# Kernel tuning notes

Measured on AMD Instinct MI355X. Metric: run time of the kernel, lower is better.

The kernel has to match this reference:

```python
import jax, jax.numpy as jnp
import numpy as np


def setup_inputs() -> dict:
    key = jax.random.key(0)
    k1, k2 = jax.random.split(key)
    z = jax.random.normal(k1, (16, 128, 32, 32), dtype=jnp.float32)
    e = jax.random.normal(k2, (8192, 128), dtype=jnp.float32)
    log_sigma = jnp.zeros((1,), dtype=jnp.float32)  # init_log_sigma = 0.0
    return {"z": z, "e": e, "log_sigma": log_sigma}


def reference(z, e, log_sigma):
    # z: [B, C, H, W] latents; e: [M, C] codebook; log_sigma: [1]
    B, C, H, W = z.shape
    zf = jnp.transpose(z, (0, 2, 3, 1)).reshape(-1, C)  # [N, C]
    N = zf.shape[0]
    M = e.shape[0]
    T = 1.0  # latent_temp default

    # squared L2 distance via expanded dot products: ||z||^2 + ||e||^2 - 2 z.e
    z_sq = jnp.sum(zf * zf, axis=1, keepdims=True)          # [N, 1]
    e_sq = jnp.sum(e * e, axis=1)[None, :]                  # [1, M]
    dist = jnp.maximum(z_sq + e_sq - 2.0 * (zf @ e.T), 0.0)  # [N, M]

    alpha = -1.0 / (2.0 * jnp.exp(log_sigma[0]) ** 2)
    A = alpha * dist / T                                     # [N, M]

    # np.log(np.e) == 1.0 in the original
    const = 0.5 * C * (2.0 * log_sigma - 1.0)                # [1]
    lse1_loss = -jnp.mean(T * jax.nn.logsumexp(A, axis=1)) + const + jnp.log(float(M))
    lse2_loss = -jnp.mean(T * jax.nn.logsumexp(A, axis=0)) + const + jnp.log(float(N))
    return lse1_loss, lse2_loss
```

## Files before the change

### kernel.cpp

```cpp
#include <hip/hip_runtime.h>
#include <hip/hip_bf16.h>

typedef unsigned short u16;
typedef __attribute__((ext_vector_type(8))) short short8;
typedef __attribute__((ext_vector_type(4))) float float4v;

#define N_ROWS 16384
#define M_COLS 8192
#define KDIM   128
#define SHIFT  64.0f
#define STRIPES 64
#define SPLITS  16
#define TILES   8

__device__ inline u16 f2bf(float f) {
  unsigned u = __builtin_bit_cast(unsigned, f);
  unsigned r = (u + 0x7fffu + ((u >> 16) & 1u)) >> 16;
  return (u16)r;
}

__global__ void prep(const float* __restrict__ z, const float* __restrict__ e,
                     u16* __restrict__ zf, u16* __restrict__ ef,
                     float* __restrict__ zsq, float* __restrict__ esq,
                     double* __restrict__ dacc, unsigned* __restrict__ dcnt) {
  if (blockIdx.x < 512) {
    const int b = blockIdx.x >> 5, h = blockIdx.x & 31;
    __shared__ float tile[128 * 33];
    __shared__ float psum[8][32];
    const float* src = z + ((size_t)b * 128 * 32 + h) * 32;
    for (int idx = threadIdx.x; idx < 4096; idx += 256) {
      int c = idx >> 5, w = idx & 31;
      tile[c * 33 + w] = src[c * 1024 + w];
    }
    __syncthreads();
    {
      int w = threadIdx.x & 31, cg = threadIdx.x >> 5;
      float s = 0.f;
#pragma unroll
      for (int cc = 0; cc < 16; ++cc) {
        float v = tile[(cg * 16 + cc) * 33 + w];
        s = fmaf(v, v, s);
      }
      psum[cg][w] = s;
    }
    for (int idx = threadIdx.x; idx < 512; idx += 256) {
      int w = idx >> 4, g = idx & 15;
      short8 v;
#pragma unroll
      for (int cc = 0; cc < 8; ++cc) v[cc] = (short)f2bf(tile[(g * 8 + cc) * 33 + w]);
      *(short8*)&zf[((size_t)b * 1024 + h * 32 + w) * 128 + g * 8] = v;
    }
    __syncthreads();
    if (threadIdx.x < 32) {
      int w = threadIdx.x;
      float s = 0.f;
#pragma unroll
      for (int cg = 0; cg < 8; ++cg) s += psum[cg][w];
      zsq[b * 1024 + h * 32 + w] = s;
    }
  } else {
    if (blockIdx.x == 512 && threadIdx.x == 0) {
      __hip_atomic_store(&dacc[0], 0.0, __ATOMIC_RELAXED, __HIP_MEMORY_SCOPE_AGENT);
      __hip_atomic_store(&dacc[1], 0.0, __ATOMIC_RELAXED, __HIP_MEMORY_SCOPE_AGENT);
      __hip_atomic_store(dcnt, 0u, __ATOMIC_RELAXED, __HIP_MEMORY_SCOPE_AGENT);
    }
    const int gw = ((blockIdx.x - 512) * 256 + threadIdx.x) >> 6;
    const int ln = threadIdx.x & 63;
    for (int r = gw; r < M_COLS; r += 512) {
      float2 v = *(const float2*)&e[r * 128 + ln * 2];
      unsigned pk = (unsigned)f2bf(v.x) | ((unsigned)f2bf(v.y) << 16);
      *(unsigned*)&ef[r * 128 + ln * 2] = pk;
      float s = fmaf(v.x, v.x, v.y * v.y);
#pragma unroll
      for (int sh = 1; sh < 64; sh <<= 1) s += __shfl_xor(s, sh);
      if (ln == 0) esq[r] = s;
    }
  }
}

__global__ __launch_bounds__(512, 4) void gemm_lse(
    const u16* __restrict__ zf, const u16* __restrict__ ef,
    const float* __restrict__ zsq, const float* __restrict__ esq,
    const float* __restrict__ log_sigma,
    float* __restrict__ rpart, float* __restrict__ cpart) {
  __shared__ __align__(16) u16 et[2][64 * 128];
  __shared__ float colacc[8][512];
  const int tid = threadIdx.x;
  const int ln = tid & 63, wv = tid >> 6;
  const int l15 = ln & 15, q = ln >> 4;
  const int stripe = blockIdx.x, split = blockIdx.y;
  const int colbase = split * 512;

  short8 af[2][4];
#pragma unroll
  for (int i = 0; i < 2; ++i)
#pragma unroll
    for (int kk = 0; kk < 4; ++kk)
      af[i][kk] = *(const short8*)(zf +
          (size_t)(stripe * 256 + wv * 32 + i * 16 + l15) * 128 + kk * 32 + q * 8);

  const float lsv = log_sigma[0];
  const float sg = __expf(lsv);
  const float alpha = -0.5f / (sg * sg);
  const float L2E = 1.44269504088896f;
  const float ca = alpha * L2E, cb = SHIFT * L2E, m2ca = -2.0f * ca;

  float4v zbl[2];
#pragma unroll
  for (int i = 0; i < 2; ++i) {
    float4v zs = *(const float4v*)(zsq + stripe * 256 + wv * 32 + i * 16 + q * 4);
#pragma unroll
    for (int r = 0; r < 4; ++r) zbl[i][r] = fmaf(ca, zs[r], cb);
  }

  float2 rs2[2][2];
#pragma unroll
  for (int i = 0; i < 2; ++i)
#pragma unroll
    for (int p = 0; p < 2; ++p) rs2[i][p] = make_float2(0.f, 0.f);

#define STAGE(tt)                                                              \
  do {                                                                         \
    const u16* efb = ef + (size_t)(colbase + (tt) * 64) * 128;                 \
    u16* dstb = et[(tt) & 1];                                                  \
    _Pragma("unroll")                                                          \
    for (int it = 0; it < 2; ++it) {                                           \
      int u = it * 512 + tid;                                                  \
      int r = u >> 4, p_ = u & 15;                                             \
      int g = p_ ^ (r & 15);                                                   \
      __builtin_amdgcn_global_load_lds(                                        \
          (const __attribute__((address_space(1))) unsigned int*)(efb + r * 128 + g * 8), \
          (__attribute__((address_space(3))) unsigned int*)(dstb + (it * 512 + wv * 64) * 8), \
          16, 0, 0);                                                           \
    }                                                                          \
  } while (0)

  STAGE(0);

  for (int t = 0; t < TILES; ++t) {
    float ebv[4];
#pragma unroll
    for (int j = 0; j < 4; ++j) ebv[j] = ca * esq[colbase + t * 64 + j * 16 + l15];

    __syncthreads();
    const u16* bb = et[t & 1];

    float4v acc[2][4];
#pragma unroll
    for (int kk = 0; kk < 4; ++kk) {
      short8 bfr[4];
      const int poff = ((kk * 4 + q) ^ l15) * 8;
#pragma unroll
      for (int j = 0; j < 4; ++j)
        bfr[j] = *(const short8*)(bb + (j * 16 + l15) * 128 + poff);
      if (kk == 0) {
#pragma unroll
        for (int i = 0; i < 2; ++i)
#pragma unroll
          for (int j = 0; j < 4; ++j)
            acc[i][j] = __builtin_amdgcn_mfma_f32_16x16x32_bf16(
                af[i][0], bfr[j], (float4v){0.f, 0.f, 0.f, 0.f}, 0, 0, 0);
      } else {
#pragma unroll
        for (int i = 0; i < 2; ++i)
#pragma unroll
          for (int j = 0; j < 4; ++j)
            acc[i][j] = __builtin_amdgcn_mfma_f32_16x16x32_bf16(
                af[i][kk], bfr[j], acc[i][j], 0, 0, 0);
      }
    }

    if (t + 1 < TILES) STAGE(t + 1);

    float2 cs2[4];
#pragma unroll
    for (int j = 0; j < 4; ++j) cs2[j] = make_float2(0.f, 0.f);

#pragma unroll
    for (int i = 0; i < 2; ++i) {
#pragma unroll
      for (int j = 0; j < 4; ++j) {
        float e0 = __builtin_amdgcn_exp2f(fmaf(acc[i][j][0], m2ca, zbl[i][0] + ebv[j]));
        float e1 = __builtin_amdgcn_exp2f(fmaf(acc[i][j][1], m2ca, zbl[i][1] + ebv[j]));
        float e2 = __builtin_amdgcn_exp2f(fmaf(acc[i][j][2], m2ca, zbl[i][2] + ebv[j]));
        float e3 = __builtin_amdgcn_exp2f(fmaf(acc[i][j][3], m2ca, zbl[i][3] + ebv[j]));
        rs2[i][0].x += e0; rs2[i][0].y += e1;
        rs2[i][1].x += e2; rs2[i][1].y += e3;
        cs2[j].x += e0 + e2; cs2[j].y += e1 + e3;
      }
    }
#pragma unroll
    for (int j = 0; j < 4; ++j) {
      float c = cs2[j].x + cs2[j].y;
      c += __shfl_xor(c, 16);
      c += __shfl_xor(c, 32);
      if (q == 0) colacc[wv][t * 64 + j * 16 + l15] = c;
    }
  }

  __syncthreads();
  {
    float s = 0.f;
#pragma unroll
    for (int w = 0; w < 8; ++w) s += colacc[w][tid];
    cpart[(size_t)stripe * M_COLS + colbase + tid] = s;
  }

#pragma unroll
  for (int i = 0; i < 2; ++i)
#pragma unroll
    for (int p = 0; p < 2; ++p)
      for (int s = 1; s < 16; s <<= 1) {
        rs2[i][p].x += __shfl_xor(rs2[i][p].x, s);
        rs2[i][p].y += __shfl_xor(rs2[i][p].y, s);
      }
  if (l15 == 0) {
#pragma unroll
    for (int i = 0; i < 2; ++i) {
      int rbase = stripe * 256 + wv * 32 + i * 16 + q * 4;
      rpart[(size_t)split * N_ROWS + rbase + 0] = rs2[i][0].x;
      rpart[(size_t)split * N_ROWS + rbase + 1] = rs2[i][0].y;
      rpart[(size_t)split * N_ROWS + rbase + 2] = rs2[i][1].x;
      rpart[(size_t)split * N_ROWS + rbase + 3] = rs2[i][1].y;
    }
  }
#undef STAGE
}

__global__ void fin(const float* __restrict__ rpart, const float* __restrict__ cpart,
                    const float* __restrict__ log_sigma,
                    double* __restrict__ dacc, unsigned* __restrict__ dcnt,
                    float* __restrict__ out) {
  const int tid = threadIdx.x, b = blockIdx.x;
  double v;
  if (b < 64) {
    int row = b * 256 + tid;
    float s = 0.f;
#pragma unroll
    for (int p = 0; p < SPLITS; ++p) s += rpart[(size_t)p * N_ROWS + row];
    v = (double)logf(s);
  } else {
    int col = (b - 64) * 256 + tid;
    float s = 0.f;
#pragma unroll
    for (int p = 0; p < STRIPES; ++p) s += cpart[(size_t)p * M_COLS + col];
    v = (double)logf(s);
  }
  __shared__ double red[256];
  red[tid] = v;
  __syncthreads();
  for (int s = 128; s > 0; s >>= 1) {
    if (tid < s) red[tid] += red[tid + s];
    __syncthreads();
  }
  if (tid == 0) {
    atomicAdd(&dacc[b < 64 ? 0 : 1], red[0]);
    __threadfence();
    unsigned ticket = atomicAdd(dcnt, 1u);
    if (ticket == 95u) {
      double s1 = atomicAdd(&dacc[0], 0.0);
      double s2 = atomicAdd(&dacc[1], 0.0);
      float lsv = log_sigma[0];
      float cst = 0.5f * 128.0f * (2.0f * lsv - 1.0f);
      out[0] = (float)(-(s1 / N_ROWS - (double)SHIFT)) + cst + logf((float)M_COLS);
      out[1] = (float)(-(s2 / M_COLS - (double)SHIFT)) + cst + logf((float)N_ROWS);
    }
  }
}

extern "C" void kernel_launch(void* const* d_in, const int* in_sizes, int n_in,
                              void* d_out, int out_size, void* d_ws, size_t ws_size,
                              hipStream_t stream) {
  const float* z  = (const float*)d_in[0];
  const float* e  = (const float*)d_in[1];
  const float* ls = (const float*)d_in[2];
  float* out = (float*)d_out;
  char* ws = (char*)d_ws;
  u16*   zf    = (u16*)ws;
  u16*   ef    = (u16*)(ws + (4u << 20));
  float* zsq   = (float*)(ws + (6u << 20));
  float* esq   = (float*)(ws + (6u << 20) + (64u << 10));
  float* rpart = (float*)(ws + (6u << 20) + (96u << 10));
  float* cpart = (float*)(ws + (7u << 20) + (96u << 10));
  double* dacc = (double*)(ws + (9u << 20) + (96u << 10));
  unsigned* dcnt = (unsigned*)(ws + (9u << 20) + (96u << 10) + 16);

  prep<<<dim3(640), dim3(256), 0, stream>>>(z, e, zf, ef, zsq, esq, dacc, dcnt);
  gemm_lse<<<dim3(STRIPES, SPLITS), dim3(512), 0, stream>>>(zf, ef, zsq, esq, ls, rpart, cpart);
  fin<<<dim3(96), dim3(256), 0, stream>>>(rpart, cpart, ls, dacc, dcnt, out);
}
```

Measured before the change: 138.2 us.

## Load whole codebook chunk into LDS upfront and double column splits

Each block now covers 256 codebook columns instead of 512, and the grid has 32 splits instead of 16. The double-buffered per-tile staging with a barrier every tile is replaced by a single up-front async load of the full 256x128 bf16 chunk into LDS, followed by one barrier. This removes the per-tile syncs and doubles the block count. In exchange, per-tile load/compute overlap is lost within a block, LDS use rises to 64KB, and the row partials the final kernel must reduce double. The workspace offsets are moved to fit the larger rpart buffer.

```diff
diff --git a/kernel.cpp b/kernel.cpp
--- a/kernel.cpp
+++ b/kernel.cpp
@@ -10,8 +10,8 @@
 #define KDIM   128
 #define SHIFT  64.0f
 #define STRIPES 64
-#define SPLITS  16
-#define TILES   8
+#define SPLITS  32
+#define CHUNKS  4
 
 __device__ inline u16 f2bf(float f) {
   unsigned u = __builtin_bit_cast(unsigned, f);
@@ -83,13 +83,27 @@
     const float* __restrict__ zsq, const float* __restrict__ esq,
     const float* __restrict__ log_sigma,
     float* __restrict__ rpart, float* __restrict__ cpart) {
-  __shared__ __align__(16) u16 et[2][64 * 128];
-  __shared__ float colacc[8][512];
+  __shared__ __align__(16) u16 et[256 * 128];
+  __shared__ float colacc[8][256];
   const int tid = threadIdx.x;
   const int ln = tid & 63, wv = tid >> 6;
   const int l15 = ln & 15, q = ln >> 4;
   const int stripe = blockIdx.x, split = blockIdx.y;
-  const int colbase = split * 512;
+  const int colbase = split * 256;
+
+  {
+    const u16* efb = ef + (size_t)colbase * 128;
+#pragma unroll
+    for (int it = 0; it < 8; ++it) {
+      int u = it * 512 + tid;
+      int r = u >> 4, p_ = u & 15;
+      int g = p_ ^ (r & 15);
+      __builtin_amdgcn_global_load_lds(
+          (const __attribute__((address_space(1))) unsigned int*)(efb + r * 128 + g * 8),
+          (__attribute__((address_space(3))) unsigned int*)(et + (it * 512 + wv * 64) * 8),
+          16, 0, 0);
+    }
+  }
 
   short8 af[2][4];
 #pragma unroll
@@ -119,31 +133,15 @@
 #pragma unroll
     for (int p = 0; p < 2; ++p) rs2[i][p] = make_float2(0.f, 0.f);
 
-#define STAGE(tt)                                                              \
-  do {                                                                         \
-    const u16* efb = ef + (size_t)(colbase + (tt) * 64) * 128;                 \
-    u16* dstb = et[(tt) & 1];                                                  \
-    _Pragma("unroll")                                                          \
-    for (int it = 0; it < 2; ++it) {                                           \
-      int u = it * 512 + tid;                                                  \
-      int r = u >> 4, p_ = u & 15;                                             \
-      int g = p_ ^ (r & 15);                                                   \
-      __builtin_amdgcn_global_load_lds(                                        \
-          (const __attribute__((address_space(1))) unsigned int*)(efb + r * 128 + g * 8), \
-          (__attribute__((address_space(3))) unsigned int*)(dstb + (it * 512 + wv * 64) * 8), \
-          16, 0, 0);                                                           \
-    }                                                                          \
-  } while (0)
-
-  STAGE(0);
-
-  for (int t = 0; t < TILES; ++t) {
+  __syncthreads();
+
+#pragma unroll
+  for (int t = 0; t < CHUNKS; ++t) {
     float ebv[4];
 #pragma unroll
     for (int j = 0; j < 4; ++j) ebv[j] = ca * esq[colbase + t * 64 + j * 16 + l15];
 
-    __syncthreads();
-    const u16* bb = et[t & 1];
+    const u16* bb = et + t * 64 * 128;
 
     float4v acc[2][4];
 #pragma unroll
@@ -169,8 +167,6 @@
                 af[i][kk], bfr[j], acc[i][j], 0, 0, 0);
       }
     }
-
-    if (t + 1 < TILES) STAGE(t + 1);
 
     float2 cs2[4];
 #pragma unroll
@@ -199,7 +195,7 @@
   }
 
   __syncthreads();
-  {
+  if (tid < 256) {
     float s = 0.f;
 #pragma unroll
     for (int w = 0; w < 8; ++w) s += colacc[w][tid];
@@ -224,7 +220,6 @@
       rpart[(size_t)split * N_ROWS + rbase + 3] = rs2[i][1].y;
     }
   }
-#undef STAGE
 }
 
 __global__ void fin(const float* __restrict__ rpart, const float* __restrict__ cpart,
@@ -281,9 +276,9 @@
   float* zsq   = (float*)(ws + (6u << 20));
   float* esq   = (float*)(ws + (6u << 20) + (64u << 10));
   float* rpart = (float*)(ws + (6u << 20) + (96u << 10));
-  float* cpart = (float*)(ws + (7u << 20) + (96u << 10));
-  double* dacc = (double*)(ws + (9u << 20) + (96u << 10));
-  unsigned* dcnt = (unsigned*)(ws + (9u << 20) + (96u << 10) + 16);
+  float* cpart = (float*)(ws + (8u << 20) + (96u << 10));
+  double* dacc = (double*)(ws + (10u << 20) + (96u << 10));
+  unsigned* dcnt = (unsigned*)(ws + (10u << 20) + (96u << 10) + 16);
 
   prep<<<dim3(640), dim3(256), 0, stream>>>(z, e, zf, ef, zsq, esq, dacc, dcnt);
   gemm_lse<<<dim3(STRIPES, SPLITS), dim3(512), 0, stream>>>(zf, ef, zsq, esq, ls, rpart, cpart);
```

Result: slower. 203.7 us (+47.4%).
